# Performance work log

Measured on AMD Instinct MI355X. Metric: run time of the kernel, lower is better.

## Reference

```python
import jax, jax.numpy as jnp
import numpy as np

TEMPERATURE = 8.0      # sqrt(d_head=64), matches init temperature
MASK_FILL = -1e32      # masked_softmax memory_efficient fill value
B, L, D = 16, 2048, 64


def setup_inputs() -> dict:
    key = jax.random.key(0)
    kq, kk, kv, kd, km = jax.random.split(key, 5)
    q = jax.random.normal(kq, (B, L, D), dtype=jnp.float32)
    k = jax.random.normal(kk, (B, L, D), dtype=jnp.float32)
    v = jax.random.normal(kv, (B, L, D), dtype=jnp.float32)
    diag_mask = jax.random.randint(kd, (B, L, L), 0, 2, dtype=jnp.int32)  # 1=keep, 0=mask
    mask = jax.random.randint(km, (B, L, L), 0, 2, dtype=jnp.int32).astype(jnp.bool_)  # True=mask out
    return {"q": q, "k": k, "v": v, "diag_mask": diag_mask, "mask": mask}


def reference(q, k, v, diag_mask, mask):
    # attn = q @ k^T / temperature   -> [B, Lq, Lk]
    attn = jnp.einsum('bqd,bkd->bqk', q, k) / TEMPERATURE
    # attn.masked_fill(mask, -inf)
    attn = jnp.where(mask, -jnp.inf, attn)
    # masked_softmax(attn, diag_mask, memory_efficient=True):
    #   masked_fill((1 - diag_mask).bool(), -1e32) then softmax
    attn = jnp.where(diag_mask == 0, MASK_FILL, attn)
    attn = jax.nn.softmax(attn, axis=-1)
    # output = attn @ v
    output = jnp.einsum('bqk,bkd->bqd', attn, v)
    return output, attn
```

## Files before the change

kernel.cpp:

```cpp
#include <hip/hip_runtime.h>
#include <math.h>

#define NB 16
#define SL 2048
#define HD 64
#define TQ 8
#define BK 64
#define NT (SL / BK)
#define SC2 0.18033688f
#define SSTRIDE 2056

typedef _Float16 half8 __attribute__((ext_vector_type(8)));
typedef float floatx4 __attribute__((ext_vector_type(4)));
typedef int intx4 __attribute__((ext_vector_type(4)));

__device__ __forceinline__ half8 load_frag_f32(const float* p) {
  floatx4 f0 = *(const floatx4*)p;
  floatx4 f1 = *(const floatx4*)(p + 4);
  half8 h;
  h[0] = (_Float16)f0[0]; h[1] = (_Float16)f0[1];
  h[2] = (_Float16)f0[2]; h[3] = (_Float16)f0[3];
  h[4] = (_Float16)f1[0]; h[5] = (_Float16)f1[1];
  h[6] = (_Float16)f1[2]; h[7] = (_Float16)f1[3];
  return h;
}

__global__ __launch_bounds__(256) void prep_pack_kernel(
    const float* __restrict__ K, const float* __restrict__ V,
    const int* __restrict__ DM, const int* __restrict__ MMk,
    _Float16* __restrict__ KH, _Float16* __restrict__ VT,
    unsigned char* __restrict__ BITS)
{
  const int bid = blockIdx.x;
  const int t   = (int)threadIdx.x;

  if (bid >= 512) {
    const size_t r0 = (size_t)(bid - 512) * 16;
    #pragma unroll 4
    for (int r = 0; r < 16; ++r) {
      const size_t off = (r0 + r) * SL + (size_t)t * 8;
      intx4 d0 = __builtin_nontemporal_load((const intx4*)(DM + off));
      intx4 d1 = __builtin_nontemporal_load((const intx4*)(DM + off + 4));
      intx4 m0 = __builtin_nontemporal_load((const intx4*)(MMk + off));
      intx4 m1 = __builtin_nontemporal_load((const intx4*)(MMk + off + 4));
      unsigned byte = 0;
      #pragma unroll
      for (int j = 0; j < 4; ++j) {
        byte |= (unsigned)((d0[j] & ~m0[j]) & 1) << j;
        byte |= (unsigned)((d1[j] & ~m1[j]) & 1) << (j + 4);
      }
      BITS[(r0 + r) * (SL / 8) + t] = (unsigned char)byte;
    }
    return;
  }

  __shared__ __align__(16) _Float16 tile[64][72];
  const int k0 = (bid & 31) * 64;
  const int b  = bid >> 5;
  const size_t base = (size_t)b * SL * HD;
  const int r  = t >> 2;
  const int cq = (t & 3) * 16;

  const float* kp = K + base + (size_t)(k0 + r) * HD + cq;
  const float* vp = V + base + (size_t)(k0 + r) * HD + cq;
  half8 kh0 = load_frag_f32(kp), kh1 = load_frag_f32(kp + 8);
  half8 vh0 = load_frag_f32(vp), vh1 = load_frag_f32(vp + 8);

  _Float16* khp = KH + base + (size_t)(k0 + r) * HD + cq;
  *(half8*)khp       = kh0;
  *(half8*)(khp + 8) = kh1;

  const int wc = cq ^ (((r >> 4) & 3) * 16);
  *(half8*)&tile[r][wc]     = vh0;
  *(half8*)&tile[r][wc + 8] = vh1;
  __syncthreads();

  const int sx = ((cq >> 4) & 3) * 16;
  half8 o0, o1;
  #pragma unroll
  for (int i = 0; i < 8; ++i) {
    o0[i] = tile[cq + i][r ^ sx];
    o1[i] = tile[cq + 8 + i][r ^ sx];
  }
  _Float16* vt = VT + (size_t)b * HD * SL + (size_t)r * SL + k0 + cq;
  *(half8*)vt       = o0;
  *(half8*)(vt + 8) = o1;
}

template <int MODE>
__global__ __launch_bounds__(512, 8) void attn_kernel(
    const float* __restrict__ Q, const float* __restrict__ K,
    const float* __restrict__ V, const _Float16* __restrict__ KH,
    const _Float16* __restrict__ VT, const unsigned char* __restrict__ BITS,
    const int* __restrict__ DM, const int* __restrict__ MMk,
    float* __restrict__ Out, float* __restrict__ Attn)
{
  const int qt    = blockIdx.x;
  const int b     = blockIdx.y;
  const int tid   = (int)threadIdx.x;
  const int w     = tid >> 6;
  const int w4    = w & 3;
  const int hf    = w >> 2;
  const int lane  = tid & 63;
  const int quad  = lane >> 4;
  const int nl    = lane & 15;

  const int qbase    = qt * TQ;
  const size_t bLD   = (size_t)b * SL * HD;
  const size_t mbase = ((size_t)b * SL + qbase) * SL;

  __shared__ __align__(16) _Float16 S[TQ * SSTRIDE];
  __shared__ unsigned bitsW[512];
  __shared__ float sinv_s[TQ];
  __shared__ float obuf[TQ][65];

  if constexpr (MODE == 2) {
    const unsigned* bp =
        (const unsigned*)(BITS + ((size_t)b * SL + qbase) * (SL / 8));
    bitsW[tid] = bp[tid];
  }

  half8 aq0, aq1;
  {
    const float* qp = Q + bLD + (size_t)(qbase + (nl & 7)) * HD + quad * 8;
    aq0 = load_frag_f32(qp);
    aq1 = load_frag_f32(qp + 32);
  }

  const int kt0 = hf * (NT / 2);
  #pragma unroll 2
  for (int kti = 0; kti < NT / 2; ++kti) {
    const int kt = kt0 + kti;
    half8 bk0, bk1;
    if constexpr (MODE >= 1) {
      const _Float16* kp = KH + bLD + (size_t)(kt * BK + w4 * 16 + nl) * HD + quad * 8;
      bk0 = *(const half8*)kp;
      bk1 = *(const half8*)(kp + 32);
    } else {
      const float* kp = K + bLD + (size_t)(kt * BK + w4 * 16 + nl) * HD + quad * 8;
      bk0 = load_frag_f32(kp);
      bk1 = load_frag_f32(kp + 32);
    }
    floatx4 acc = {0.f, 0.f, 0.f, 0.f};
    acc = __builtin_amdgcn_mfma_f32_16x16x32_f16(aq0, bk0, acc, 0, 0, 0);
    acc = __builtin_amdgcn_mfma_f32_16x16x32_f16(aq1, bk1, acc, 0, 0, 0);
    const int col = kt * BK + w4 * 16 + nl;
    if (quad < 2) {
      #pragma unroll
      for (int r = 0; r < 4; ++r)
        S[(quad * 4 + r) * SSTRIDE + col] = (_Float16)(acc[r] * SC2);
    }
  }
  __syncthreads();

  _Float16* srow = &S[w * SSTRIDE];
  float sum = 0.f;
  if constexpr (MODE == 2) {
    const unsigned char* bl = (const unsigned char*)bitsW;
    #pragma unroll
    for (int it = 0; it < 4; ++it) {
      const int c = it * 512 + lane * 8;
      const unsigned kb = bl[w * 256 + it * 64 + lane];
      half8 s8 = *(const half8*)(srow + c);
      half8 e8;
      #pragma unroll
      for (int j = 0; j < 4; ++j) {
        const float e0 = (kb & (1u << j))       ? __builtin_amdgcn_exp2f((float)s8[j])     : 0.f;
        const float e1 = (kb & (1u << (j + 4))) ? __builtin_amdgcn_exp2f((float)s8[j + 4]) : 0.f;
        sum += e0 + e1;
        e8[j]     = (_Float16)e0;
        e8[j + 4] = (_Float16)e1;
      }
      *(half8*)(srow + c) = e8;
    }
  } else {
    const int* dmr = DM  + mbase + (size_t)w * SL;
    const int* mkr = MMk + mbase + (size_t)w * SL;
    #pragma unroll
    for (int it = 0; it < 4; ++it) {
      const int c = it * 512 + lane * 8;
      intx4 d0 = __builtin_nontemporal_load((const intx4*)(dmr + c));
      intx4 d1 = __builtin_nontemporal_load((const intx4*)(dmr + c + 4));
      intx4 m0 = __builtin_nontemporal_load((const intx4*)(mkr + c));
      intx4 m1 = __builtin_nontemporal_load((const intx4*)(mkr + c + 4));
      half8 s8 = *(const half8*)(srow + c);
      half8 e8;
      #pragma unroll
      for (int j = 0; j < 4; ++j) {
        const int keep0 = d0[j] & ~m0[j];
        const int keep1 = d1[j] & ~m1[j];
        const float e0 = keep0 ? __builtin_amdgcn_exp2f((float)s8[j])     : 0.f;
        const float e1 = keep1 ? __builtin_amdgcn_exp2f((float)s8[j + 4]) : 0.f;
        sum += e0 + e1;
        e8[j]     = (_Float16)e0;
        e8[j + 4] = (_Float16)e1;
      }
      *(half8*)(srow + c) = e8;
    }
  }
  #pragma unroll
  for (int off = 1; off < 64; off <<= 1)
    sum += __shfl_xor(sum, off, 64);
  if (lane == 0) sinv_s[w] = (sum > 0.f) ? 1.f / sum : 0.f;
  __syncthreads();

  const float isr = sinv_s[w];
  float* arow = Attn + mbase + (size_t)w * SL;
  floatx4 oacc = {0.f, 0.f, 0.f, 0.f};
  #pragma unroll
  for (int kti = 0; kti < NT / 2; ++kti) {
    const int kt = kt0 + kti;
    half8 ap0 = *(const half8*)(&S[(nl & 7) * SSTRIDE + kt * BK + quad * 8]);
    half8 ap1 = *(const half8*)(&S[(nl & 7) * SSTRIDE + kt * BK + quad * 8 + 32]);
    half8 bv0, bv1;
    if constexpr (MODE >= 1) {
      const _Float16* vp = VT + bLD + (size_t)(w4 * 16 + nl) * SL + kt * BK + quad * 8;
      bv0 = *(const half8*)vp;
      bv1 = *(const half8*)(vp + 32);
    } else {
      const float* vp = V + bLD + (size_t)(kt * BK + quad * 8) * HD + w4 * 16 + nl;
      #pragma unroll
      for (int j = 0; j < 8; ++j) {
        bv0[j] = (_Float16)vp[(size_t)j * HD];
        bv1[j] = (_Float16)vp[(size_t)(j + 32) * HD];
      }
    }
    oacc = __builtin_amdgcn_mfma_f32_16x16x32_f16(ap0, bv0, oacc, 0, 0, 0);
    oacc = __builtin_amdgcn_mfma_f32_16x16x32_f16(ap1, bv1, oacc, 0, 0, 0);
    if ((kti & 3) == 0) {
      const int c = (kti >> 2) * 512 + lane * 8;
      half8 e8v = *(const half8*)(srow + c);
      floatx4 o0, o1;
      #pragma unroll
      for (int j = 0; j < 4; ++j) {
        o0[j] = (float)e8v[j]     * isr;
        o1[j] = (float)e8v[j + 4] * isr;
      }
      __builtin_nontemporal_store(o0, (floatx4*)(arow + c));
      __builtin_nontemporal_store(o1, (floatx4*)(arow + c + 4));
    }
  }

  if (hf == 1 && quad < 2) {
    #pragma unroll
    for (int r = 0; r < 4; ++r)
      obuf[quad * 4 + r][w4 * 16 + nl] = oacc[r];
  }
  __syncthreads();
  if (hf == 0 && quad < 2) {
    float* op = Out + ((size_t)b * SL + qbase) * HD;
    #pragma unroll
    for (int r = 0; r < 4; ++r) {
      const int row = quad * 4 + r;
      op[(size_t)row * HD + w4 * 16 + nl] =
          (oacc[r] + obuf[row][w4 * 16 + nl]) * sinv_s[row];
    }
  }
}

extern "C" void kernel_launch(void* const* d_in, const int* in_sizes, int n_in,
                              void* d_out, int out_size, void* d_ws, size_t ws_size,
                              hipStream_t stream) {
  const float* Q  = (const float*)d_in[0];
  const float* K  = (const float*)d_in[1];
  const float* V  = (const float*)d_in[2];
  const int* DM   = (const int*)d_in[3];
  const int* MMk  = (const int*)d_in[4];
  float* Out  = (float*)d_out;
  float* Attn = (float*)d_out + (size_t)NB * SL * HD;
  dim3 grid(SL / TQ, NB);

  const size_t needKV   = (size_t)2 * NB * SL * HD * sizeof(_Float16);
  const size_t needBits = (size_t)NB * SL * (SL / 8);
  if (d_ws != nullptr && ws_size >= needKV + needBits) {
    _Float16* KH = (_Float16*)d_ws;
    _Float16* VT = KH + (size_t)NB * SL * HD;
    unsigned char* BITS = (unsigned char*)(VT + (size_t)NB * SL * HD);
    prep_pack_kernel<<<dim3(512 + 2048), 256, 0, stream>>>(K, V, DM, MMk, KH, VT, BITS);
    attn_kernel<2><<<grid, 512, 0, stream>>>(Q, K, V, KH, VT, BITS, DM, MMk, Out, Attn);
  } else if (d_ws != nullptr && ws_size >= needKV) {
    _Float16* KH = (_Float16*)d_ws;
    _Float16* VT = KH + (size_t)NB * SL * HD;
    prep_pack_kernel<<<dim3(512), 256, 0, stream>>>(K, V, DM, MMk, KH, VT, nullptr);
    attn_kernel<1><<<grid, 512, 0, stream>>>(Q, K, V, KH, VT, nullptr, DM, MMk, Out, Attn);
  } else {
    attn_kernel<0><<<grid, 512, 0, stream>>>(Q, K, V, nullptr, nullptr, nullptr, DM, MMk, Out, Attn);
  }
}
```

Before: 853.1 us.

## Process 32 query rows per block to reuse K/V fragments across two MFMA tiles

Raises the query tile from 8 to 32 rows per block. Each wave now computes two 16-row MFMA tiles that share the same K and V fragments, and the softmax and attn-write phases are remapped so 16 threads cover each row. This removes the wasted half of each 16x16 MFMA (previously only 8 rows were used) and cuts K/V reloads per query by four. In exchange, LDS use grows to about 130KB per block and the launch-bounds occupancy hint drops from 8 to 2, which lowers latency hiding in a kernel dominated by mask reads and attention writes.

```diff
diff --git a/kernel.cpp b/kernel.cpp
--- a/kernel.cpp
+++ b/kernel.cpp
@@ -4,7 +4,7 @@
 #define NB 16
 #define SL 2048
 #define HD 64
-#define TQ 8
+#define TQ 32
 #define BK 64
 #define NT (SL / BK)
 #define SC2 0.18033688f
@@ -88,7 +88,7 @@
 }
 
 template <int MODE>
-__global__ __launch_bounds__(512, 8) void attn_kernel(
+__global__ __launch_bounds__(512, 2) void attn_kernel(
     const float* __restrict__ Q, const float* __restrict__ K,
     const float* __restrict__ V, const _Float16* __restrict__ KH,
     const _Float16* __restrict__ VT, const unsigned char* __restrict__ BITS,
@@ -104,27 +104,31 @@
   const int lane  = tid & 63;
   const int quad  = lane >> 4;
   const int nl    = lane & 15;
+  const int row32 = tid >> 4;
+  const int ci    = tid & 15;
 
   const int qbase    = qt * TQ;
   const size_t bLD   = (size_t)b * SL * HD;
   const size_t mbase = ((size_t)b * SL + qbase) * SL;
 
   __shared__ __align__(16) _Float16 S[TQ * SSTRIDE];
-  __shared__ unsigned bitsW[512];
+  __shared__ __align__(16) unsigned char bitsB[TQ * 256];
   __shared__ float sinv_s[TQ];
   __shared__ float obuf[TQ][65];
 
   if constexpr (MODE == 2) {
-    const unsigned* bp =
-        (const unsigned*)(BITS + ((size_t)b * SL + qbase) * (SL / 8));
-    bitsW[tid] = bp[tid];
-  }
-
-  half8 aq0, aq1;
+    const intx4* bp = (const intx4*)(BITS + ((size_t)b * SL + qbase) * (SL / 8));
+    ((intx4*)bitsB)[tid] = bp[tid];
+  }
+
+  half8 aq0, aq1, aq2, aq3;
   {
-    const float* qp = Q + bLD + (size_t)(qbase + (nl & 7)) * HD + quad * 8;
+    const float* qp = Q + bLD + (size_t)(qbase + nl) * HD + quad * 8;
     aq0 = load_frag_f32(qp);
     aq1 = load_frag_f32(qp + 32);
+    const float* qp2 = Q + bLD + (size_t)(qbase + 16 + nl) * HD + quad * 8;
+    aq2 = load_frag_f32(qp2);
+    aq3 = load_frag_f32(qp2 + 32);
   }
 
   const int kt0 = hf * (NT / 2);
@@ -141,26 +145,28 @@
       bk0 = load_frag_f32(kp);
       bk1 = load_frag_f32(kp + 32);
     }
-    floatx4 acc = {0.f, 0.f, 0.f, 0.f};
-    acc = __builtin_amdgcn_mfma_f32_16x16x32_f16(aq0, bk0, acc, 0, 0, 0);
-    acc = __builtin_amdgcn_mfma_f32_16x16x32_f16(aq1, bk1, acc, 0, 0, 0);
+    floatx4 acc0 = {0.f, 0.f, 0.f, 0.f};
+    floatx4 acc1 = {0.f, 0.f, 0.f, 0.f};
+    acc0 = __builtin_amdgcn_mfma_f32_16x16x32_f16(aq0, bk0, acc0, 0, 0, 0);
+    acc0 = __builtin_amdgcn_mfma_f32_16x16x32_f16(aq1, bk1, acc0, 0, 0, 0);
+    acc1 = __builtin_amdgcn_mfma_f32_16x16x32_f16(aq2, bk0, acc1, 0, 0, 0);
+    acc1 = __builtin_amdgcn_mfma_f32_16x16x32_f16(aq3, bk1, acc1, 0, 0, 0);
     const int col = kt * BK + w4 * 16 + nl;
-    if (quad < 2) {
-      #pragma unroll
-      for (int r = 0; r < 4; ++r)
-        S[(quad * 4 + r) * SSTRIDE + col] = (_Float16)(acc[r] * SC2);
+    #pragma unroll
+    for (int r = 0; r < 4; ++r) {
+      S[(quad * 4 + r) * SSTRIDE + col]        = (_Float16)(acc0[r] * SC2);
+      S[(16 + quad * 4 + r) * SSTRIDE + col]   = (_Float16)(acc1[r] * SC2);
     }
   }
   __syncthreads();
 
-  _Float16* srow = &S[w * SSTRIDE];
+  _Float16* srow = &S[row32 * SSTRIDE];
   float sum = 0.f;
   if constexpr (MODE == 2) {
-    const unsigned char* bl = (const unsigned char*)bitsW;
-    #pragma unroll
-    for (int it = 0; it < 4; ++it) {
-      const int c = it * 512 + lane * 8;
-      const unsigned kb = bl[w * 256 + it * 64 + lane];
+    #pragma unroll 4
+    for (int it = 0; it < 16; ++it) {
+      const int c = it * 128 + ci * 8;
+      const unsigned kb = bitsB[row32 * 256 + it * 16 + ci];
       half8 s8 = *(const half8*)(srow + c);
       half8 e8;
       #pragma unroll
@@ -174,11 +180,11 @@
       *(half8*)(srow + c) = e8;
     }
   } else {
-    const int* dmr = DM  + mbase + (size_t)w * SL;
-    const int* mkr = MMk + mbase + (size_t)w * SL;
-    #pragma unroll
-    for (int it = 0; it < 4; ++it) {
-      const int c = it * 512 + lane * 8;
+    const int* dmr = DM  + mbase + (size_t)row32 * SL;
+    const int* mkr = MMk + mbase + (size_t)row32 * SL;
+    #pragma unroll 4
+    for (int it = 0; it < 16; ++it) {
+      const int c = it * 128 + ci * 8;
       intx4 d0 = __builtin_nontemporal_load((const intx4*)(dmr + c));
       intx4 d1 = __builtin_nontemporal_load((const intx4*)(dmr + c + 4));
       intx4 m0 = __builtin_nontemporal_load((const intx4*)(mkr + c));
@@ -199,19 +205,22 @@
     }
   }
   #pragma unroll
-  for (int off = 1; off < 64; off <<= 1)
+  for (int off = 1; off < 16; off <<= 1)
     sum += __shfl_xor(sum, off, 64);
-  if (lane == 0) sinv_s[w] = (sum > 0.f) ? 1.f / sum : 0.f;
+  if (ci == 0) sinv_s[row32] = (sum > 0.f) ? 1.f / sum : 0.f;
   __syncthreads();
 
-  const float isr = sinv_s[w];
-  float* arow = Attn + mbase + (size_t)w * SL;
-  floatx4 oacc = {0.f, 0.f, 0.f, 0.f};
-  #pragma unroll
+  const float isr = sinv_s[row32];
+  float* arow = Attn + mbase + (size_t)row32 * SL;
+  floatx4 oacc0 = {0.f, 0.f, 0.f, 0.f};
+  floatx4 oacc1 = {0.f, 0.f, 0.f, 0.f};
+  #pragma unroll 2
   for (int kti = 0; kti < NT / 2; ++kti) {
     const int kt = kt0 + kti;
-    half8 ap0 = *(const half8*)(&S[(nl & 7) * SSTRIDE + kt * BK + quad * 8]);
-    half8 ap1 = *(const half8*)(&S[(nl & 7) * SSTRIDE + kt * BK + quad * 8 + 32]);
+    half8 ap0 = *(const half8*)(&S[nl * SSTRIDE + kt * BK + quad * 8]);
+    half8 ap1 = *(const half8*)(&S[nl * SSTRIDE + kt * BK + quad * 8 + 32]);
+    half8 ap2 = *(const half8*)(&S[(16 + nl) * SSTRIDE + kt * BK + quad * 8]);
+    half8 ap3 = *(const half8*)(&S[(16 + nl) * SSTRIDE + kt * BK + quad * 8 + 32]);
     half8 bv0, bv1;
     if constexpr (MODE >= 1) {
       const _Float16* vp = VT + bLD + (size_t)(w4 * 16 + nl) * SL + kt * BK + quad * 8;
@@ -225,10 +234,12 @@
         bv1[j] = (_Float16)vp[(size_t)(j + 32) * HD];
       }
     }
-    oacc = __builtin_amdgcn_mfma_f32_16x16x32_f16(ap0, bv0, oacc, 0, 0, 0);
-    oacc = __builtin_amdgcn_mfma_f32_16x16x32_f16(ap1, bv1, oacc, 0, 0, 0);
-    if ((kti & 3) == 0) {
-      const int c = (kti >> 2) * 512 + lane * 8;
+    oacc0 = __builtin_amdgcn_mfma_f32_16x16x32_f16(ap0, bv0, oacc0, 0, 0, 0);
+    oacc0 = __builtin_amdgcn_mfma_f32_16x16x32_f16(ap1, bv1, oacc0, 0, 0, 0);
+    oacc1 = __builtin_amdgcn_mfma_f32_16x16x32_f16(ap2, bv0, oacc1, 0, 0, 0);
+    oacc1 = __builtin_amdgcn_mfma_f32_16x16x32_f16(ap3, bv1, oacc1, 0, 0, 0);
+    {
+      const int c = kti * 128 + ci * 8;
       half8 e8v = *(const half8*)(srow + c);
       floatx4 o0, o1;
       #pragma unroll
@@ -241,19 +252,24 @@
     }
   }
 
-  if (hf == 1 && quad < 2) {
+  if (hf == 1) {
     #pragma unroll
-    for (int r = 0; r < 4; ++r)
-      obuf[quad * 4 + r][w4 * 16 + nl] = oacc[r];
+    for (int r = 0; r < 4; ++r) {
+      obuf[quad * 4 + r][w4 * 16 + nl]      = oacc0[r];
+      obuf[16 + quad * 4 + r][w4 * 16 + nl] = oacc1[r];
+    }
   }
   __syncthreads();
-  if (hf == 0 && quad < 2) {
+  if (hf == 0) {
     float* op = Out + ((size_t)b * SL + qbase) * HD;
     #pragma unroll
     for (int r = 0; r < 4; ++r) {
       const int row = quad * 4 + r;
       op[(size_t)row * HD + w4 * 16 + nl] =
-          (oacc[r] + obuf[row][w4 * 16 + nl]) * sinv_s[row];
+          (oacc0[r] + obuf[row][w4 * 16 + nl]) * sinv_s[row];
+      const int row2 = 16 + quad * 4 + r;
+      op[(size_t)row2 * HD + w4 * 16 + nl] =
+          (oacc1[r] + obuf[row2][w4 * 16 + nl]) * sinv_s[row2];
     }
   }
 }
```

Result: faster. 706.3 us (-17.2%).
